# Kernel tuning notes

Measured on AMD Instinct MI355X. Metric: run time of the kernel, lower is better.

Reference implementation:

```python
import jax, jax.numpy as jnp
import numpy as np

N_FILTRATIONS = 24
TEMPERATURE = 0.15
H1_WEIGHT = 0.5
LAMBDA_TOPO = 0.1


def setup_inputs() -> dict:
    key = jax.random.key(0)
    embeddings = jax.random.normal(key, (4096, 512), dtype=jnp.float32)
    return {"embeddings": embeddings, "step": 0}


def _landscape_loss(embeddings):
    N = embeddings.shape[0]
    emb = embeddings.astype(jnp.float32)
    # pairwise euclidean distances (torch.cdist p=2), safe sqrt for grad at 0
    sq = jnp.sum(emb * emb, axis=1)
    d2 = sq[:, None] + sq[None, :] - 2.0 * (emb @ emb.T)
    d2 = jnp.maximum(d2, 0.0)
    pos = d2 > 1e-12
    dist = jnp.where(pos, jnp.sqrt(jnp.where(pos, d2, 1.0)), 0.0)
    eye = jnp.eye(N, dtype=jnp.float32)
    dist = dist + eye * 1e9  # [N, N], diag pushed to 'infinity'
    off = dist < 1e8
    # thresholds come from .item() in torch -> no grad through them
    d_min = jax.lax.stop_gradient(jnp.min(jnp.where(off, dist, jnp.inf)))
    d_max = jax.lax.stop_gradient(
        jnp.maximum(jnp.max(jnp.where(off, dist, -jnp.inf)), d_min + 1e-4))
    thresholds = jnp.linspace(d_min, d_max, N_FILTRATIONS)

    one_minus_eye = 1.0 - eye

    def step_fn(carry, thresh):
        adj = jax.nn.sigmoid((thresh - dist) / TEMPERATURE) * one_minus_eye
        deg = jnp.clip(jnp.sum(adj, axis=-1), 1e-6, None)
        n_isolated = jnp.sum((deg < 0.5).astype(jnp.float32))  # H0 proxy
        n_edges_soft = jnp.sum(adj) / 2.0
        n_excess = jax.nn.relu(n_edges_soft - (N - 1)) / N  # H1 proxy
        return carry, (n_isolated, n_excess)

    _, (h0, h1) = jax.lax.scan(step_fn, None, thresholds)
    h0_loss = jnp.mean(h0[-8:])
    h1_loss = jnp.mean(h1)
    total = h0_loss + H1_WEIGHT * h1_loss
    return total * LAMBDA_TOPO


def reference(embeddings, step) -> jnp.ndarray:
    # warmup_steps = 0, so the warmup skip branch never triggers;
    # N == max_points, so no subsampling.
    return _landscape_loss(embeddings)
```

## Files before the change

kernel.cpp:

```cpp
#include <hip/hip_runtime.h>
#include <stdint.h>

typedef float f32x4 __attribute__((ext_vector_type(4)));
typedef short s16x8 __attribute__((ext_vector_type(8)));
typedef unsigned short us4 __attribute__((ext_vector_type(4)));

#define NPTS 4096
#define DDIM 512
#define NF   24
#define NBLK 32
#define NB   2048

#define OFF_SQ  4194304
#define OFF_MM  4210688
#define OFF_DEG 4210752
#define OFF_D   4603968
#define OFF_H   38158400ULL
#define WS_A    54935616ULL

typedef __attribute__((address_space(1))) void gvoid;
typedef __attribute__((address_space(3))) void svoid;
#define GLD16(gp, lp) __builtin_amdgcn_global_load_lds((gvoid*)(gp), (svoid*)(lp), 16, 0, 0)

static __device__ __forceinline__ ushort f2h(float x) {
    _Float16 h = (_Float16)x;
    return __builtin_bit_cast(unsigned short, h);
}
static __device__ __forceinline__ float h2f(ushort u) {
    return (float)__builtin_bit_cast(_Float16, u);
}

__global__ __launch_bounds__(256) void k_init(float* __restrict__ deg,
                                              unsigned* __restrict__ mm) {
    int i = blockIdx.x * 256 + threadIdx.x;
    if (i < NPTS * NF) deg[i] = 0.0f;
    if (i == 0) { mm[0] = 0x7F7FFFFFu; mm[1] = 0u; }
}

__global__ __launch_bounds__(256) void k_convert(const float* __restrict__ in,
                                                 ushort* __restrict__ Eb,
                                                 float* __restrict__ sq,
                                                 float* __restrict__ acc32,
                                                 unsigned* __restrict__ mm) {
    if (blockIdx.x == 0) {
        if (threadIdx.x < 32) acc32[threadIdx.x] = 0.0f;
        else if (threadIdx.x == 32) mm[0] = 0x7F7FFFFFu;
        else if (threadIdx.x == 33) mm[1] = 0u;
    }
    const int w = threadIdx.x >> 6, lane = threadIdx.x & 63;
    const int row = blockIdx.x * 4 + w;
    const float* src = in + (size_t)row * DDIM + lane * 8;
    float4 a = ((const float4*)src)[0];
    float4 b = ((const float4*)src)[1];
    float v[8] = {a.x, a.y, a.z, a.w, b.x, b.y, b.z, b.w};
    unsigned u[8];
    float ss = 0.0f;
#pragma unroll
    for (int i = 0; i < 8; ++i) {
        ss += v[i] * v[i];
        unsigned bits = __float_as_uint(v[i]);
        u[i] = (bits + 0x7FFFu + ((bits >> 16) & 1u)) >> 16;
    }
    uint4 pk;
    pk.x = u[0] | (u[1] << 16);
    pk.y = u[2] | (u[3] << 16);
    pk.z = u[4] | (u[5] << 16);
    pk.w = u[6] | (u[7] << 16);
    *(uint4*)(Eb + (size_t)row * DDIM + lane * 8) = pk;
#pragma unroll
    for (int s = 1; s < 64; s <<= 1) ss += __shfl_xor(ss, s);
    if (lane == 0) sq[row] = ss;
}

__global__ __launch_bounds__(256) void k_gram_bk64(const ushort* __restrict__ Eb,
                                                   const float* __restrict__ sq,
                                                   unsigned* __restrict__ mm,
                                                   ushort* __restrict__ D2h) {
    __shared__ __align__(16) ushort SM[32768];
    __shared__ float sqr[128], sqc[128], red[8];
    char* SMb = (char*)SM;
    const int tid = threadIdx.x;
    const int w = tid >> 6, lane = tid & 63, g = lane >> 4, l15 = lane & 15;
    const int wr = w >> 1, wc = w & 1;

    int bid = (blockIdx.x & 7) * 66 + (blockIdx.x >> 3);
    int rb = 0, pre = 0;
    while (pre + (NBLK - rb) <= bid) { pre += NBLK - rb; ++rb; }
    const int cb = rb + (bid - pre);

    if (tid < 128) sqr[tid] = sq[rb * 128 + tid];
    else           sqc[tid - 128] = sq[cb * 128 + (tid - 128)];

    f32x4 acc[4][4];
#pragma unroll
    for (int i = 0; i < 4; ++i)
#pragma unroll
        for (int j = 0; j < 4; ++j) acc[i][j] = (f32x4){0.f, 0.f, 0.f, 0.f};

    const int srow_off = lane >> 3, slch = lane & 7;

#define STAGE64(buf, kk)                                                        \
    {                                                                           \
        const int k0_ = (kk) * 64;                                              \
        _Pragma("unroll")                                                       \
        for (int i_ = 0; i_ < 4; ++i_) {                                        \
            const int r_  = w * 32 + i_ * 8 + srow_off;                         \
            const int ch_ = slch ^ (r_ & 7);                                    \
            GLD16(Eb + (size_t)(rb * 128 + r_) * DDIM + k0_ + ch_ * 8,          \
                  SMb + (buf) * 16384 + (w * 32 + i_ * 8) * 128);               \
            GLD16(Eb + (size_t)(cb * 128 + r_) * DDIM + k0_ + ch_ * 8,          \
                  SMb + 32768 + (buf) * 16384 + (w * 32 + i_ * 8) * 128);       \
        }                                                                       \
    }

    STAGE64(0, 0);
    int cur = 0;
#pragma unroll 1
    for (int kk = 0; kk < 8; ++kk) {
        __syncthreads();
        if (kk < 7) STAGE64(cur ^ 1, kk + 1);
        const char* Ac = SMb + cur * 16384;
        const char* Bc = SMb + 32768 + cur * 16384;
#pragma unroll
        for (int ks = 0; ks < 2; ++ks) {
            s16x8 rf[4], cf[4];
#pragma unroll
            for (int i = 0; i < 4; ++i) {
                const int r = wr * 64 + i * 16 + l15;
                const int slot = (ks * 4 + g) ^ (r & 7);
                rf[i] = *(const s16x8*)(Ac + r * 128 + slot * 16);
            }
#pragma unroll
            for (int j = 0; j < 4; ++j) {
                const int r = wc * 64 + j * 16 + l15;
                const int slot = (ks * 4 + g) ^ (r & 7);
                cf[j] = *(const s16x8*)(Bc + r * 128 + slot * 16);
            }
#pragma unroll
            for (int i = 0; i < 4; ++i)
#pragma unroll
                for (int j = 0; j < 4; ++j)
                    acc[i][j] = __builtin_amdgcn_mfma_f32_16x16x32_bf16(
                        cf[j], rf[i], acc[i][j], 0, 0, 0);
        }
        cur ^= 1;
    }
    __syncthreads();

    ushort* T = SM;
    float mn = 3.4e38f, mx = 0.0f;
#pragma unroll
    for (int i = 0; i < 4; ++i) {
        const int lr = wr * 64 + i * 16 + l15;
        const int trow = rb * 128 + lr;
        const float srv = sqr[lr];
#pragma unroll
        for (int j = 0; j < 4; ++j) {
            const int c0 = wc * 64 + j * 16 + g * 4;
            const int tc0 = cb * 128 + c0;
            ushort h[4];
#pragma unroll
            for (int m = 0; m < 4; ++m) {
                float d2 = srv + sqc[c0 + m] - 2.0f * acc[i][j][m];
                d2 = fmaxf(d2, 0.0f);
                bool diag = (tc0 + m == trow);
                mn = diag ? mn : fminf(mn, d2);
                mx = diag ? mx : fmaxf(mx, d2);
                h[m] = f2h(diag ? 6.0e4f : d2);
            }
            us4 pk4 = {h[0], h[1], h[2], h[3]};
            *(us4*)(T + lr * 136 + c0) = pk4;
        }
    }
#pragma unroll
    for (int s = 1; s < 64; s <<= 1) {
        mn = fminf(mn, __shfl_xor(mn, s));
        mx = fmaxf(mx, __shfl_xor(mx, s));
    }
    if (lane == 0) { red[w] = mn; red[4 + w] = mx; }
    __syncthreads();
    if (tid == 0) {
        mn = fminf(fminf(red[0], red[1]), fminf(red[2], red[3]));
        mx = fmaxf(fmaxf(red[4], red[5]), fmaxf(red[6], red[7]));
        atomicMin(&mm[0], __float_as_uint(mn));
        atomicMax(&mm[1], __float_as_uint(mx));
    }
#pragma unroll
    for (int j = 0; j < 8; ++j) {
        const int c = j * 256 + tid;
        const int row = c >> 4, col8 = (c & 15) * 8;
        uint4 v = *(const uint4*)(T + row * 136 + col8);
        *(uint4*)(D2h + (size_t)(rb * 128 + row) * NPTS + cb * 128 + col8) = v;
    }
    if (rb != cb) {
        __syncthreads();
#pragma unroll
        for (int i = 0; i < 4; ++i) {
            const int lr = wr * 64 + i * 16 + l15;
            const float srv = sqr[lr];
#pragma unroll
            for (int j = 0; j < 4; ++j) {
                const int c0 = wc * 64 + j * 16 + g * 4;
#pragma unroll
                for (int m = 0; m < 4; ++m) {
                    float d2 = srv + sqc[c0 + m] - 2.0f * acc[i][j][m];
                    d2 = fmaxf(d2, 0.0f);
                    T[(c0 + m) * 136 + lr] = f2h(d2);
                }
            }
        }
        __syncthreads();
#pragma unroll
        for (int j2 = 0; j2 < 8; ++j2) {
            const int c = j2 * 256 + tid;
            const int row = c >> 4, col8 = (c & 15) * 8;
            uint4 v = *(const uint4*)(T + row * 136 + col8);
            *(uint4*)(D2h + (size_t)(cb * 128 + row) * NPTS + rb * 128 + col8) = v;
        }
    }
}

__global__ __launch_bounds__(256) void k_hist4(const ushort* __restrict__ D2h,
                                               const unsigned* __restrict__ mm,
                                               ushort* __restrict__ H) {
    __shared__ unsigned Hs[4][NB + 4];
    const int tid = threadIdx.x, w = tid >> 6, lane = tid & 63;
    const int row0 = blockIdx.x * 4;
    const int row = row0 + w;
    for (int i = tid; i < 4 * (NB + 4); i += 256) ((unsigned*)Hs)[i] = 0u;
    const float d2min = __uint_as_float(mm[0]);
    const float d2max = __uint_as_float(mm[1]);
    const float sc = (float)NB / fmaxf(d2max - d2min, 1e-6f);
    __syncthreads();
    const uint4* Dv = (const uint4*)(D2h + (size_t)row * NPTS);
    unsigned* hr = Hs[w];
#pragma unroll
    for (int it = 0; it < 8; ++it) {
        uint4 pk = Dv[it * 64 + lane];
        unsigned pw[4] = {pk.x, pk.y, pk.z, pk.w};
#pragma unroll
        for (int i = 0; i < 4; ++i) {
            float a = h2f((ushort)(pw[i] & 0xFFFFu));
            float b = h2f((ushort)(pw[i] >> 16));
            if (a < 3.0e4f) {
                int ba = (int)fminf(fmaxf((a - d2min) * sc, 0.0f), (float)(NB - 1));
                atomicAdd(&hr[ba], 1u);
            }
            if (b < 3.0e4f) {
                int bb = (int)fminf(fmaxf((b - d2min) * sc, 0.0f), (float)(NB - 1));
                atomicAdd(&hr[bb], 1u);
            }
        }
    }
    __syncthreads();
    unsigned* Ho = (unsigned*)(H + (size_t)row0 * NB);
    for (int i = tid; i < 4 * (NB / 2); i += 256) {
        const int r = i >> 10, pw_ = i & 1023;
        unsigned lo = Hs[r][2 * pw_], hi = Hs[r][2 * pw_ + 1];
        Ho[r * (NB / 2) + pw_] = (lo & 0xFFFFu) | (hi << 16);
    }
}

__global__ __launch_bounds__(512) void k_dot(const ushort* __restrict__ H,
                                             const unsigned* __restrict__ mm,
                                             float* __restrict__ acc32) {
    __shared__ float Wl[4][NB];
    __shared__ float degb[8][NF];
    const int tid = threadIdx.x;
    const int wid = tid >> 6, lane = tid & 63;
    const int row = blockIdx.x * 8 + wid;

    const float d2min = __uint_as_float(mm[0]);
    const float d2max = __uint_as_float(mm[1]);
    const float bw    = fmaxf(d2max - d2min, 1e-6f) / (float)NB;
    const float d_min = d2min > 1e-12f ? sqrtf(d2min) : 0.0f;
    const float d_mx  = d2max > 1e-12f ? sqrtf(d2max) : 0.0f;
    const float d_max = fmaxf(d_mx, d_min + 1e-4f);
    const float stp   = (d_max - d_min) / 23.0f;
    const float S2L   = (1.0f / 0.15f) * 1.44269504f;
    const float Ds2   = stp * S2L;
    const float R     = exp2f(-Ds2);
    const float LIM   = 1073741824.0f;

    float hv[32];
    const ushort* Hr = H + (size_t)row * NB;
#pragma unroll
    for (int j = 0; j < 8; ++j) {
        uint2 pk = *(const uint2*)(Hr + j * 256 + lane * 4);
        hv[j * 4 + 0] = (float)(pk.x & 0xFFFFu);
        hv[j * 4 + 1] = (float)(pk.x >> 16);
        hv[j * 4 + 2] = (float)(pk.y & 0xFFFFu);
        hv[j * 4 + 3] = (float)(pk.y >> 16);
    }

    float e4[4];
#pragma unroll
    for (int q = 0; q < 4; ++q) {
        const int b = tid * 4 + q;
        const float d2c = d2min + ((float)b + 0.5f) * bw;
        const float db = sqrtf(fmaxf(d2c, 0.0f));
        e4[q] = exp2f(fminf((db - d_min) * S2L, 125.0f));
    }

#pragma unroll 1
    for (int ph = 0; ph < 6; ++ph) {
        __syncthreads();
#pragma unroll
        for (int k = 0; k < 4; ++k) {
            f32x4 sg;
#pragma unroll
            for (int q = 0; q < 4; ++q) {
                sg[q] = __builtin_amdgcn_rcpf(1.0f + fminf(e4[q], LIM));
                e4[q] *= R;
            }
            *(f32x4*)(&Wl[k][tid * 4]) = sg;
        }
        __syncthreads();
        float dacc[4];
#pragma unroll
        for (int k = 0; k < 4; ++k) {
            const float* Wr = &Wl[k][0];
            float s = 0.0f;
#pragma unroll
            for (int j = 0; j < 8; ++j) {
                const f32x4 wv = *(const f32x4*)(Wr + j * 256 + lane * 4);
                s += hv[j*4+0]*wv[0] + hv[j*4+1]*wv[1] + hv[j*4+2]*wv[2] + hv[j*4+3]*wv[3];
            }
            dacc[k] = s;
        }
#pragma unroll
        for (int k = 0; k < 4; ++k)
#pragma unroll
            for (int o = 1; o < 64; o <<= 1) dacc[k] += __shfl_xor(dacc[k], o);
        if (lane == 0) {
#pragma unroll
            for (int k = 0; k < 4; ++k) degb[wid][ph * 4 + k] = dacc[k];
        }
    }
    __syncthreads();
    if (tid < NF) {
        float s = 0.0f;
#pragma unroll
        for (int r = 0; r < 8; ++r) s += degb[r][tid];
        atomicAdd(&acc32[tid], s);
    } else if (tid < 32) {
        const int k = 16 + (tid - NF);
        float c = 0.0f;
#pragma unroll
        for (int r = 0; r < 8; ++r) c += (degb[r][k] < 0.5f) ? 1.0f : 0.0f;
        atomicAdd(&acc32[tid], c);
    }
}

__global__ __launch_bounds__(64) void k_final2(const float* __restrict__ acc32,
                                               float* __restrict__ out) {
    if (threadIdx.x == 0) {
        float h1 = 0.0f;
#pragma unroll
        for (int k = 0; k < NF; ++k)
            h1 += fmaxf(acc32[k] * 0.5f - (float)(NPTS - 1), 0.0f) * (1.0f / (float)NPTS);
        float h0 = 0.0f;
#pragma unroll
        for (int k = 0; k < 8; ++k) h0 += acc32[NF + k];
        out[0] = (h0 * 0.125f + 0.5f * (h1 * (1.0f / 24.0f))) * 0.1f;
    }
}

__device__ __forceinline__ void gram_tile(const ushort* __restrict__ Eb, int rb, int cb,
                                          ushort* As, ushort* Bs, f32x4 acc[2][8]) {
    const int tid = threadIdx.x;
    const int w = tid >> 6, lane = tid & 63, g = lane >> 4, l15 = lane & 15;
#pragma unroll 1
    for (int kk = 0; kk < DDIM / 32; ++kk) {
        const int k0 = kk * 32;
        __syncthreads();
#pragma unroll
        for (int it = 0; it < 2; ++it) {
            int li  = it * 256 + tid;
            int row = li >> 2, ch = li & 3;
            uint4 va = *(const uint4*)(Eb + (size_t)(rb * 128 + row) * DDIM + k0 + ch * 8);
            uint4 vb = *(const uint4*)(Eb + (size_t)(cb * 128 + row) * DDIM + k0 + ch * 8);
            *(uint4*)(As + row * 32 + ch * 8) = va;
            *(uint4*)(Bs + row * 32 + ch * 8) = vb;
        }
        __syncthreads();
        s16x8 rf0 = *(const s16x8*)(As + (w * 32 + 0 * 16 + l15) * 32 + g * 8);
        s16x8 rf1 = *(const s16x8*)(As + (w * 32 + 1 * 16 + l15) * 32 + g * 8);
#pragma unroll
        for (int bj = 0; bj < 8; ++bj) {
            s16x8 cf = *(const s16x8*)(Bs + (bj * 16 + l15) * 32 + g * 8);
            acc[0][bj] = __builtin_amdgcn_mfma_f32_16x16x32_bf16(cf, rf0, acc[0][bj], 0, 0, 0);
            acc[1][bj] = __builtin_amdgcn_mfma_f32_16x16x32_bf16(cf, rf1, acc[1][bj], 0, 0, 0);
        }
    }
}

__global__ __launch_bounds__(256) void k_minmax(const ushort* __restrict__ Eb,
                                                const float* __restrict__ sq,
                                                unsigned* __restrict__ mm) {
    const int rb = blockIdx.y, cb = blockIdx.x;
    if (cb < rb) return;
    __shared__ ushort As[128 * 32], Bs[128 * 32];
    __shared__ float sqr[128], sqc[128];
    __shared__ float red[8];
    const int tid = threadIdx.x;
    if (tid < 128) sqr[tid] = sq[rb * 128 + tid];
    else           sqc[tid - 128] = sq[cb * 128 + (tid - 128)];
    f32x4 acc[2][8];
#pragma unroll
    for (int bi = 0; bi < 2; ++bi)
#pragma unroll
        for (int bj = 0; bj < 8; ++bj) acc[bi][bj] = (f32x4){0.f, 0.f, 0.f, 0.f};
    gram_tile(Eb, rb, cb, As, Bs, acc);
    const int w = tid >> 6, lane = tid & 63, g = lane >> 4, l15 = lane & 15;
    const float sr0 = sqr[w * 32 + l15], sr1 = sqr[w * 32 + 16 + l15];
    float mn = 3.4e38f, mx = 0.0f;
#pragma unroll
    for (int bi = 0; bi < 2; ++bi)
#pragma unroll
        for (int bj = 0; bj < 8; ++bj)
#pragma unroll
            for (int m = 0; m < 4; ++m) {
                int tr = w * 32 + bi * 16 + l15;
                int tc = bj * 16 + g * 4 + m;
                float d2 = (bi ? sr1 : sr0) + sqc[tc] - 2.0f * acc[bi][bj][m];
                d2 = fmaxf(d2, 0.0f);
                bool diag = (rb == cb) && (tr == tc);
                mn = diag ? mn : fminf(mn, d2);
                mx = diag ? mx : fmaxf(mx, d2);
            }
#pragma unroll
    for (int s = 1; s < 64; s <<= 1) {
        mn = fminf(mn, __shfl_xor(mn, s));
        mx = fmaxf(mx, __shfl_xor(mx, s));
    }
    if (lane == 0) { red[w] = mn; red[4 + w] = mx; }
    __syncthreads();
    if (tid == 0) {
        mn = fminf(fminf(red[0], red[1]), fminf(red[2], red[3]));
        mx = fmaxf(fmaxf(red[4], red[5]), fmaxf(red[6], red[7]));
        atomicMin(&mm[0], __float_as_uint(mn));
        atomicMax(&mm[1], __float_as_uint(mx));
    }
}

__global__ __launch_bounds__(256) void k_accum2(const ushort* __restrict__ Eb,
                                                const float* __restrict__ sq,
                                                const unsigned* __restrict__ mm,
                                                float* __restrict__ deg) {
    const int rb = blockIdx.y, cb = blockIdx.x;
    __shared__ ushort As[128 * 32], Bs[128 * 32];
    __shared__ float sqr[128], sqc[128];
    __shared__ float degr[128][NF];
    const int tid = threadIdx.x;
    if (tid < 128) sqr[tid] = sq[rb * 128 + tid];
    else           sqc[tid - 128] = sq[cb * 128 + (tid - 128)];
    for (int i = tid; i < 128 * NF; i += 256) ((float*)degr)[i] = 0.0f;
    f32x4 acc[2][8];
#pragma unroll
    for (int bi = 0; bi < 2; ++bi)
#pragma unroll
        for (int bj = 0; bj < 8; ++bj) acc[bi][bj] = (f32x4){0.f, 0.f, 0.f, 0.f};
    gram_tile(Eb, rb, cb, As, Bs, acc);
    const int w = tid >> 6, lane = tid & 63, g = lane >> 4, l15 = lane & 15;

    const float dmin2 = __uint_as_float(mm[0]);
    const float dmax2 = __uint_as_float(mm[1]);
    const float d_min = dmin2 > 1e-12f ? sqrtf(dmin2) : 0.0f;
    const float d_mx  = dmax2 > 1e-12f ? sqrtf(dmax2) : 0.0f;
    const float d_max = fmaxf(d_mx, d_min + 1e-4f);
    const float stp   = (d_max - d_min) / 23.0f;
    const float S2L   = (1.0f / 0.15f) * 1.44269504f;
    const float Ds2   = stp * S2L;
    const float R     = exp2f(-Ds2);
    const float LIM   = 1073741824.0f;
    const float ECAP  = 125.0f;

    const float sr0 = sqr[w * 32 + l15], sr1 = sqr[w * 32 + 16 + l15];
    f32x4 ee[2][8];
#pragma unroll
    for (int bi = 0; bi < 2; ++bi)
#pragma unroll
        for (int bj = 0; bj < 8; ++bj)
#pragma unroll
            for (int m = 0; m < 4; ++m) {
                int tr = w * 32 + bi * 16 + l15;
                int tc = bj * 16 + g * 4 + m;
                float d2 = (bi ? sr1 : sr0) + sqc[tc] - 2.0f * acc[bi][bj][m];
                d2 = fmaxf(d2, 0.0f);
                float d = d2 > 1e-12f ? sqrtf(d2) : 0.0f;
                if (rb == cb && tr == tc) d = 1e9f;
                ee[bi][bj][m] = exp2f(fminf((d - d_min) * S2L, ECAP));
            }

#pragma unroll 1
    for (int t = 0; t < NF; ++t) {
        float rs0 = 0.0f, rs1 = 0.0f;
#pragma unroll
        for (int bj = 0; bj < 8; ++bj) {
            {
                f32x4 q = ee[0][bj];
                float A  = 1.0f + fminf(q.x, LIM), B  = 1.0f + fminf(q.y, LIM);
                float Cq = 1.0f + fminf(q.z, LIM), Dq = 1.0f + fminf(q.w, LIM);
                float sAB = A + B,  sCD = Cq + Dq;
                float pAB = A * B,  pCD = Cq * Dq;
                rs0 += (sAB * pCD + sCD * pAB) * __builtin_amdgcn_rcpf(pAB * pCD);
                ee[0][bj] = q * R;
            }
            {
                f32x4 q = ee[1][bj];
                float A  = 1.0f + fminf(q.x, LIM), B  = 1.0f + fminf(q.y, LIM);
                float Cq = 1.0f + fminf(q.z, LIM), Dq = 1.0f + fminf(q.w, LIM);
                float sAB = A + B,  sCD = Cq + Dq;
                float pAB = A * B,  pCD = Cq * Dq;
                rs1 += (sAB * pCD + sCD * pAB) * __builtin_amdgcn_rcpf(pAB * pCD);
                ee[1][bj] = q * R;
            }
        }
        rs0 += __shfl_xor(rs0, 16); rs0 += __shfl_xor(rs0, 32);
        rs1 += __shfl_xor(rs1, 16); rs1 += __shfl_xor(rs1, 32);
        if (g == 0) {
            degr[w * 32 + l15][t]      += rs0;
            degr[w * 32 + 16 + l15][t] += rs1;
        }
    }
    __syncthreads();
    for (int i = tid; i < 128 * NF; i += 256) {
        int r = i / NF, t = i % NF;
        atomicAdd(&deg[(size_t)(rb * 128 + r) * NF + t], degr[r][t]);
    }
}

__global__ __launch_bounds__(256) void k_final(const float* __restrict__ deg,
                                               float* __restrict__ out) {
    const int tid = threadIdx.x;
    float s[NF], cnt[8];
#pragma unroll
    for (int t = 0; t < NF; ++t) s[t] = 0.0f;
#pragma unroll
    for (int k = 0; k < 8; ++k) cnt[k] = 0.0f;
    for (int i = tid; i < NPTS; i += 256) {
        const float* row = deg + (size_t)i * NF;
#pragma unroll
        for (int t = 0; t < NF; ++t) {
            float v = row[t];
            s[t] += v;
            if (t >= 16) cnt[t - 16] += (v < 0.5f) ? 1.0f : 0.0f;
        }
    }
#pragma unroll
    for (int t = 0; t < NF; ++t)
#pragma unroll
        for (int o = 1; o < 64; o <<= 1) s[t] += __shfl_xor(s[t], o);
#pragma unroll
    for (int k = 0; k < 8; ++k)
#pragma unroll
        for (int o = 1; o < 64; o <<= 1) cnt[k] += __shfl_xor(cnt[k], o);
    __shared__ float red[4][32];
    const int w = tid >> 6, lane = tid & 63;
    if (lane == 0) {
#pragma unroll
        for (int t = 0; t < NF; ++t) red[w][t] = s[t];
#pragma unroll
        for (int k = 0; k < 8; ++k) red[w][NF + k] = cnt[k];
    }
    __syncthreads();
    if (tid == 0) {
        float h0 = 0.0f, h1 = 0.0f;
#pragma unroll
        for (int t = 0; t < NF; ++t) {
            float S = red[0][t] + red[1][t] + red[2][t] + red[3][t];
            float edges = S * 0.5f;
            h1 += fmaxf(edges - (float)(NPTS - 1), 0.0f) / (float)NPTS;
        }
#pragma unroll
        for (int k = 0; k < 8; ++k)
            h0 += red[0][NF + k] + red[1][NF + k] + red[2][NF + k] + red[3][NF + k];
        h0 *= (1.0f / 8.0f);
        h1 *= (1.0f / 24.0f);
        out[0] = (h0 + 0.5f * h1) * 0.1f;
    }
}

extern "C" void kernel_launch(void* const* d_in, const int* in_sizes, int n_in,
                              void* d_out, int out_size, void* d_ws, size_t ws_size,
                              hipStream_t stream) {
    (void)in_sizes; (void)n_in; (void)out_size;
    const float* emb = (const float*)d_in[0];
    uint8_t* ws = (uint8_t*)d_ws;
    ushort*   Eb  = (ushort*)(ws);
    float*    sqv = (float*)(ws + OFF_SQ);
    unsigned* mm  = (unsigned*)(ws + OFF_MM);
    float*    deg = (float*)(ws + OFF_DEG);
    ushort*   D2h = (ushort*)(ws + OFF_D);
    ushort*   H   = (ushort*)(ws + OFF_H);
    float*    out = (float*)d_out;
    const bool bigws = (ws_size >= WS_A);

    if (bigws) {
        k_convert <<<dim3(NPTS / 4),              dim3(256), 0, stream>>>(emb, Eb, sqv, deg, mm);
        k_gram_bk64<<<dim3(NBLK * (NBLK + 1) / 2), dim3(256), 0, stream>>>(Eb, sqv, mm, D2h);
        k_hist4   <<<dim3(NPTS / 4),              dim3(256), 0, stream>>>(D2h, mm, H);
        k_dot     <<<dim3(NPTS / 8),              dim3(512), 0, stream>>>(H, mm, deg);
        k_final2  <<<dim3(1),                     dim3(64),  0, stream>>>(deg, out);
    } else {
        k_init   <<<dim3(384),      dim3(256), 0, stream>>>(deg, mm);
        k_convert<<<dim3(NPTS / 4), dim3(256), 0, stream>>>(emb, Eb, sqv, deg, mm);
        k_minmax <<<dim3(32, 32),   dim3(256), 0, stream>>>(Eb, sqv, mm);
        k_accum2 <<<dim3(32, 32),   dim3(256), 0, stream>>>(Eb, sqv, mm, deg);
        k_final  <<<dim3(1),        dim3(256), 0, stream>>>(deg, out);
    }
}
```

Before: 83.09 us.

## Fuse histogram and sigmoid-weighted dot kernels, precompute fp16 weight table

Merges the per-row distance histogram kernel and the threshold dot-product kernel into one, so histograms stay in shared memory instead of round-tripping through global memory as packed 16-bit counts. The sigmoid weights for all 24 thresholds are now computed once by a small separate kernel into an fp16 table, then staged into LDS per phase, replacing the per-block recomputation with a recurrence. This removes one global write/read pass and redundant exp/rcp work, at the cost of fp16 weight precision and a smaller 4-row block for the dot phase.

```diff
diff --git a/kernel.cpp b/kernel.cpp
--- a/kernel.cpp
+++ b/kernel.cpp
@@ -4,6 +4,7 @@
 typedef float f32x4 __attribute__((ext_vector_type(4)));
 typedef short s16x8 __attribute__((ext_vector_type(8)));
 typedef unsigned short us4 __attribute__((ext_vector_type(4)));
+typedef unsigned short us8 __attribute__((ext_vector_type(8)));
 
 #define NPTS 4096
 #define DDIM 512
@@ -220,56 +221,9 @@
     }
 }
 
-__global__ __launch_bounds__(256) void k_hist4(const ushort* __restrict__ D2h,
-                                               const unsigned* __restrict__ mm,
-                                               ushort* __restrict__ H) {
-    __shared__ unsigned Hs[4][NB + 4];
-    const int tid = threadIdx.x, w = tid >> 6, lane = tid & 63;
-    const int row0 = blockIdx.x * 4;
-    const int row = row0 + w;
-    for (int i = tid; i < 4 * (NB + 4); i += 256) ((unsigned*)Hs)[i] = 0u;
-    const float d2min = __uint_as_float(mm[0]);
-    const float d2max = __uint_as_float(mm[1]);
-    const float sc = (float)NB / fmaxf(d2max - d2min, 1e-6f);
-    __syncthreads();
-    const uint4* Dv = (const uint4*)(D2h + (size_t)row * NPTS);
-    unsigned* hr = Hs[w];
-#pragma unroll
-    for (int it = 0; it < 8; ++it) {
-        uint4 pk = Dv[it * 64 + lane];
-        unsigned pw[4] = {pk.x, pk.y, pk.z, pk.w};
-#pragma unroll
-        for (int i = 0; i < 4; ++i) {
-            float a = h2f((ushort)(pw[i] & 0xFFFFu));
-            float b = h2f((ushort)(pw[i] >> 16));
-            if (a < 3.0e4f) {
-                int ba = (int)fminf(fmaxf((a - d2min) * sc, 0.0f), (float)(NB - 1));
-                atomicAdd(&hr[ba], 1u);
-            }
-            if (b < 3.0e4f) {
-                int bb = (int)fminf(fmaxf((b - d2min) * sc, 0.0f), (float)(NB - 1));
-                atomicAdd(&hr[bb], 1u);
-            }
-        }
-    }
-    __syncthreads();
-    unsigned* Ho = (unsigned*)(H + (size_t)row0 * NB);
-    for (int i = tid; i < 4 * (NB / 2); i += 256) {
-        const int r = i >> 10, pw_ = i & 1023;
-        unsigned lo = Hs[r][2 * pw_], hi = Hs[r][2 * pw_ + 1];
-        Ho[r * (NB / 2) + pw_] = (lo & 0xFFFFu) | (hi << 16);
-    }
-}
-
-__global__ __launch_bounds__(512) void k_dot(const ushort* __restrict__ H,
-                                             const unsigned* __restrict__ mm,
-                                             float* __restrict__ acc32) {
-    __shared__ float Wl[4][NB];
-    __shared__ float degb[8][NF];
-    const int tid = threadIdx.x;
-    const int wid = tid >> 6, lane = tid & 63;
-    const int row = blockIdx.x * 8 + wid;
-
+__global__ __launch_bounds__(256) void k_wgen(const unsigned* __restrict__ mm,
+                                              ushort* __restrict__ W16) {
+    const int b = blockIdx.x * 256 + threadIdx.x;
     const float d2min = __uint_as_float(mm[0]);
     const float d2max = __uint_as_float(mm[1]);
     const float bw    = fmaxf(d2max - d2min, 1e-6f) / (float)NB;
@@ -278,76 +232,103 @@
     const float d_max = fmaxf(d_mx, d_min + 1e-4f);
     const float stp   = (d_max - d_min) / 23.0f;
     const float S2L   = (1.0f / 0.15f) * 1.44269504f;
-    const float Ds2   = stp * S2L;
-    const float R     = exp2f(-Ds2);
     const float LIM   = 1073741824.0f;
+    const float d2c = d2min + ((float)b + 0.5f) * bw;
+    const float db  = sqrtf(fmaxf(d2c, 0.0f));
+#pragma unroll
+    for (int k = 0; k < NF; ++k) {
+        const float t = d_min + (float)k * stp;
+        const float e = exp2f(fminf((db - t) * S2L, 125.0f));
+        const float sg = __builtin_amdgcn_rcpf(1.0f + fminf(e, LIM));
+        W16[k * NB + b] = f2h(sg);
+    }
+}
+
+__global__ __launch_bounds__(256) void k_histdot(const ushort* __restrict__ D2h,
+                                                 const ushort* __restrict__ W16,
+                                                 const unsigned* __restrict__ mm,
+                                                 float* __restrict__ acc32) {
+    __shared__ unsigned Hs[4][NB + 4];
+    __shared__ ushort Wl[4][NB];
+    __shared__ float degb[4][NF];
+    const int tid = threadIdx.x, w = tid >> 6, lane = tid & 63;
+    const int row = blockIdx.x * 4 + w;
+
+    for (int i = tid; i < 4 * (NB + 4); i += 256) ((unsigned*)Hs)[i] = 0u;
+    const float d2min = __uint_as_float(mm[0]);
+    const float d2max = __uint_as_float(mm[1]);
+    const float sc = (float)NB / fmaxf(d2max - d2min, 1e-6f);
+    __syncthreads();
+
+    const uint4* Dv = (const uint4*)(D2h + (size_t)row * NPTS);
+    unsigned* hr = Hs[w];
+#pragma unroll
+    for (int it = 0; it < 8; ++it) {
+        uint4 pk = Dv[it * 64 + lane];
+        unsigned pw[4] = {pk.x, pk.y, pk.z, pk.w};
+#pragma unroll
+        for (int i = 0; i < 4; ++i) {
+            float a = h2f((ushort)(pw[i] & 0xFFFFu));
+            float b = h2f((ushort)(pw[i] >> 16));
+            if (a < 3.0e4f) {
+                int ba = (int)fminf(fmaxf((a - d2min) * sc, 0.0f), (float)(NB - 1));
+                atomicAdd(&hr[ba], 1u);
+            }
+            if (b < 3.0e4f) {
+                int bb = (int)fminf(fmaxf((b - d2min) * sc, 0.0f), (float)(NB - 1));
+                atomicAdd(&hr[bb], 1u);
+            }
+        }
+    }
+    __syncthreads();
 
     float hv[32];
-    const ushort* Hr = H + (size_t)row * NB;
-#pragma unroll
-    for (int j = 0; j < 8; ++j) {
-        uint2 pk = *(const uint2*)(Hr + j * 256 + lane * 4);
-        hv[j * 4 + 0] = (float)(pk.x & 0xFFFFu);
-        hv[j * 4 + 1] = (float)(pk.x >> 16);
-        hv[j * 4 + 2] = (float)(pk.y & 0xFFFFu);
-        hv[j * 4 + 3] = (float)(pk.y >> 16);
-    }
-
-    float e4[4];
-#pragma unroll
-    for (int q = 0; q < 4; ++q) {
-        const int b = tid * 4 + q;
-        const float d2c = d2min + ((float)b + 0.5f) * bw;
-        const float db = sqrtf(fmaxf(d2c, 0.0f));
-        e4[q] = exp2f(fminf((db - d_min) * S2L, 125.0f));
+#pragma unroll
+    for (int j = 0; j < 4; ++j) {
+#pragma unroll
+        for (int p = 0; p < 2; ++p) {
+            uint4 q = *(const uint4*)(&Hs[w][j * 512 + lane * 8 + p * 4]);
+            hv[j * 8 + p * 4 + 0] = (float)q.x;
+            hv[j * 8 + p * 4 + 1] = (float)q.y;
+            hv[j * 8 + p * 4 + 2] = (float)q.z;
+            hv[j * 8 + p * 4 + 3] = (float)q.w;
+        }
     }
 
 #pragma unroll 1
     for (int ph = 0; ph < 6; ++ph) {
         __syncthreads();
 #pragma unroll
-        for (int k = 0; k < 4; ++k) {
-            f32x4 sg;
-#pragma unroll
-            for (int q = 0; q < 4; ++q) {
-                sg[q] = __builtin_amdgcn_rcpf(1.0f + fminf(e4[q], LIM));
-                e4[q] *= R;
-            }
-            *(f32x4*)(&Wl[k][tid * 4]) = sg;
-        }
-        __syncthreads();
-        float dacc[4];
-#pragma unroll
-        for (int k = 0; k < 4; ++k) {
-            const float* Wr = &Wl[k][0];
+        for (int k4 = 0; k4 < 4; ++k4)
+            *(uint4*)(&Wl[k4][tid * 8]) =
+                *(const uint4*)(W16 + (size_t)(ph * 4 + k4) * NB + tid * 8);
+        __syncthreads();
+#pragma unroll
+        for (int k4 = 0; k4 < 4; ++k4) {
             float s = 0.0f;
 #pragma unroll
-            for (int j = 0; j < 8; ++j) {
-                const f32x4 wv = *(const f32x4*)(Wr + j * 256 + lane * 4);
-                s += hv[j*4+0]*wv[0] + hv[j*4+1]*wv[1] + hv[j*4+2]*wv[2] + hv[j*4+3]*wv[3];
-            }
-            dacc[k] = s;
-        }
-#pragma unroll
-        for (int k = 0; k < 4; ++k)
-#pragma unroll
-            for (int o = 1; o < 64; o <<= 1) dacc[k] += __shfl_xor(dacc[k], o);
-        if (lane == 0) {
-#pragma unroll
-            for (int k = 0; k < 4; ++k) degb[wid][ph * 4 + k] = dacc[k];
+            for (int j = 0; j < 4; ++j) {
+                us8 wv = *(const us8*)(&Wl[k4][j * 512 + lane * 8]);
+#pragma unroll
+                for (int i = 0; i < 8; ++i)
+                    s += hv[j * 8 + i] * h2f(wv[i]);
+            }
+#pragma unroll
+            for (int o = 1; o < 64; o <<= 1) s += __shfl_xor(s, o);
+            if (lane == 0) degb[w][ph * 4 + k4] = s;
         }
     }
     __syncthreads();
     if (tid < NF) {
         float s = 0.0f;
 #pragma unroll
-        for (int r = 0; r < 8; ++r) s += degb[r][tid];
+        for (int r = 0; r < 4; ++r) s += degb[r][tid];
         atomicAdd(&acc32[tid], s);
     } else if (tid < 32) {
         const int k = 16 + (tid - NF);
         float c = 0.0f;
 #pragma unroll
-        for (int r = 0; r < 8; ++r) c += (degb[r][k] < 0.5f) ? 1.0f : 0.0f;
+        for (int r = 0; r < 4; ++r) c += (degb[r][k] < 0.5f) ? 1.0f : 0.0f;
         atomicAdd(&acc32[tid], c);
     }
 }
@@ -593,16 +574,16 @@
     unsigned* mm  = (unsigned*)(ws + OFF_MM);
     float*    deg = (float*)(ws + OFF_DEG);
     ushort*   D2h = (ushort*)(ws + OFF_D);
-    ushort*   H   = (ushort*)(ws + OFF_H);
+    ushort*   W16 = (ushort*)(ws + OFF_H);
     float*    out = (float*)d_out;
     const bool bigws = (ws_size >= WS_A);
 
     if (bigws) {
-        k_convert <<<dim3(NPTS / 4),              dim3(256), 0, stream>>>(emb, Eb, sqv, deg, mm);
-        k_gram_bk64<<<dim3(NBLK * (NBLK + 1) / 2), dim3(256), 0, stream>>>(Eb, sqv, mm, D2h);
-        k_hist4   <<<dim3(NPTS / 4),              dim3(256), 0, stream>>>(D2h, mm, H);
-        k_dot     <<<dim3(NPTS / 8),              dim3(512), 0, stream>>>(H, mm, deg);
-        k_final2  <<<dim3(1),                     dim3(64),  0, stream>>>(deg, out);
+        k_convert  <<<dim3(NPTS / 4),               dim3(256), 0, stream>>>(emb, Eb, sqv, deg, mm);
+        k_gram_bk64<<<dim3(NBLK * (NBLK + 1) / 2),  dim3(256), 0, stream>>>(Eb, sqv, mm, D2h);
+        k_wgen     <<<dim3(NB / 256),               dim3(256), 0, stream>>>(mm, W16);
+        k_histdot  <<<dim3(NPTS / 4),               dim3(256), 0, stream>>>(D2h, W16, mm, deg);
+        k_final2   <<<dim3(1),                      dim3(64),  0, stream>>>(deg, out);
     } else {
         k_init   <<<dim3(384),      dim3(256), 0, stream>>>(deg, mm);
         k_convert<<<dim3(NPTS / 4), dim3(256), 0, stream>>>(emb, Eb, sqv, deg, mm);
```

Result: slower. 94.16 us (+13.3%).
